# Optimization experiments

Hardware: AMD Instinct MI355X
Metric: run time of the kernel (lower is better)

Reference implementation:

```python
import jax, jax.numpy as jnp
import numpy as np

B, T = 1, 2048
N_HEAD = 16
N_KV_HEAD = 16
N_EMBD = 1024
HEAD_DIM = N_EMBD // N_HEAD  # 64
HD8 = HEAD_DIM // 8          # 8 octonion blocks per head
EPS_RMS = 1e-6


def qconj(q):
    return q * jnp.array([1.0, -1.0, -1.0, -1.0], dtype=q.dtype)


def qmul(q1, q2):
    # Hamilton product, (...,4) x (...,4) -> (...,4)
    w1, x1, y1, z1 = (q1[..., 0], q1[..., 1], q1[..., 2], q1[..., 3])
    w2, x2, y2, z2 = (q2[..., 0], q2[..., 1], q2[..., 2], q2[..., 3])
    return jnp.stack([
        w1 * w2 - x1 * x2 - y1 * y2 - z1 * z2,
        w1 * x2 + x1 * w2 + y1 * z2 - z1 * y2,
        w1 * y2 - x1 * z2 + y1 * w2 + z1 * x2,
        w1 * z2 + x1 * y2 - y1 * x2 + z1 * w2,
    ], axis=-1)


def omul(o1, o2):
    # Cayley-Dickson octonion product, (...,8)
    a, b = o1[..., :4], o1[..., 4:]
    c, d = o2[..., :4], o2[..., 4:]
    first = qmul(a, c) - qmul(qconj(d), b)
    second = qmul(d, a) + qmul(b, qconj(c))
    return jnp.concatenate([first, second], axis=-1)


def oconj(o):
    return jnp.concatenate([qconj(o[..., :4]), -o[..., 4:]], axis=-1)


# Octonion multiplication structure constants: omul(x, y)[k] = x[a] y[p] C[a,p,k]
_EYE8 = jnp.eye(8, dtype=jnp.float32)
C_OCT = jax.vmap(lambda ei: jax.vmap(lambda ej: omul(ei, ej))(_EYE8))(_EYE8)  # (8,8,8)
# Trilinear tensor for omul(omul(q, kc), v):  T3[a,p,q,k] = sum_e C[a,p,e] C[e,q,k]
T3 = jnp.einsum('ape,eqk->apqk', C_OCT, C_OCT)  # (8,8,8,8)


def apply_rotary_emb(x, cos, sin):
    # x: (B, T, H, hd); cos/sin: (1, T, 1, hd//2)
    d = x.shape[-1] // 2
    x1, x2 = x[..., :d], x[..., d:]
    y1 = x1 * cos + x2 * sin
    y2 = x2 * cos - x1 * sin
    return jnp.concatenate([y1, y2], axis=-1)


def rms_norm(x):
    return x * jax.lax.rsqrt(jnp.mean(x * x, axis=-1, keepdims=True) + EPS_RMS)


def setup_inputs() -> dict:
    key = jax.random.key(0)
    ks = jax.random.split(key, 7)
    x = jax.random.normal(ks[0], (B, T, N_EMBD), dtype=jnp.float32)
    cos = jax.random.uniform(ks[1], (1, T, 1, HEAD_DIM // 2), dtype=jnp.float32)
    sin = jax.random.uniform(ks[2], (1, T, 1, HEAD_DIM // 2), dtype=jnp.float32)
    s = 0.02
    Wq = jax.random.normal(ks[3], (N_HEAD * HEAD_DIM, N_EMBD), dtype=jnp.float32) * s
    Wk = jax.random.normal(ks[4], (N_KV_HEAD * HEAD_DIM, N_EMBD), dtype=jnp.float32) * s
    Wv = jax.random.normal(ks[5], (N_KV_HEAD * HEAD_DIM, N_EMBD), dtype=jnp.float32) * s
    Wo = jax.random.normal(ks[6], (N_EMBD, N_EMBD), dtype=jnp.float32) * s
    return {"x": x, "cos": cos, "sin": sin, "Wq": Wq, "Wk": Wk, "Wv": Wv, "Wo": Wo}


def reference(x, cos, sin, Wq, Wk, Wv, Wo):
    Bx, Tx, Cx = x.shape
    q = (x @ Wq.T).reshape(Bx, Tx, N_HEAD, HEAD_DIM)
    k = (x @ Wk.T).reshape(Bx, Tx, N_KV_HEAD, HEAD_DIM)
    v = (x @ Wv.T).reshape(Bx, Tx, N_KV_HEAD, HEAD_DIM)
    q = rms_norm(apply_rotary_emb(q, cos, sin))
    k = rms_norm(apply_rotary_emb(k, cos, sin))
    q = q.transpose(0, 2, 1, 3)  # (B,H,T,hd)
    k = k.transpose(0, 2, 1, 3)
    v = v.transpose(0, 2, 1, 3)

    q_o = q.reshape(Bx, N_HEAD, Tx, HD8, 8)
    k_o = k.reshape(Bx, N_KV_HEAD, Tx, HD8, 8)
    v_o = v.reshape(Bx, N_KV_HEAD, Tx, HD8, 8)
    # F.normalize(p=2, dim=-1): divide by max(||.||, 1e-12)
    k_o = k_o / jnp.maximum(jnp.linalg.norm(k_o, axis=-1, keepdims=True), 1e-12)

    # Scores use the (pre-octonion-normalized) rotary+rms k
    scores = jnp.einsum('bhid,bhjd->bhij', q, k) * (HEAD_DIM ** -0.5)
    mask = jnp.tril(jnp.ones((Tx, Tx), dtype=bool))
    scores = jnp.where(mask, scores, -jnp.inf)
    probs = jax.nn.softmax(scores, axis=-1)  # (B,H,Tq,Tk)

    # y_i = sum_j p_ij * omul(omul(q_i, oconj(k_j)), v_j)
    # omul is bilinear, so pull the j-sum inside:
    # y_i[k] = q_i[a] * T3[a,p,c,k] * (sum_j p_ij kc_j[p] v_j[c])
    kc = oconj(k_o)                                              # (B,H,Tk,M,8)
    KV = jnp.einsum('bhjmp,bhjmq->bhjmpq', kc, v_o)              # (B,H,Tk,M,8,8)
    Z = jnp.einsum('bhij,bhjmpq->bhimpq', probs, KV)             # (B,H,Tq,M,8,8)
    y_o = jnp.einsum('bhima,apqk,bhimpq->bhimk', q_o, T3, Z)     # (B,H,Tq,M,8)

    y = y_o.reshape(Bx, N_HEAD, Tx, HEAD_DIM).transpose(0, 2, 1, 3).reshape(Bx, Tx, Cx)
    return y @ Wo.T
```

## Files before the change

### kernel.cpp

```cpp
#include <hip/hip_runtime.h>

typedef unsigned short u16;
typedef unsigned int u32;

#define T_SEQ 2048
#define NHEAD 16
#define HDIM 64
#define CDIM 1024
#define W_HSTR (512*2048)
#define Z_HSTR (2048*512)
#define P_HSTR 2228224
#define P_TILE 16384

#define SGBITS 0xB2D8741EACC66A00ULL

#define EXP2C 0.18033688011112042f

typedef _Float16 f16x8 __attribute__((ext_vector_type(8)));
typedef float f32x4 __attribute__((ext_vector_type(4)));

__device__ __forceinline__ float h2f(u16 u) { _Float16 h; __builtin_memcpy(&h, &u, 2); return (float)h; }
__device__ __forceinline__ u16 f2h(float f) { _Float16 h = (_Float16)f; u16 u; __builtin_memcpy(&u, &h, 2); return u; }
__device__ __forceinline__ u32 pk(float a, float b) { return (u32)f2h(a) | ((u32)f2h(b) << 16); }

__device__ __forceinline__ void gload16(const u16* g, u16* l) {
    __builtin_amdgcn_global_load_lds((const __attribute__((address_space(1))) u32*)g,
                                     (__attribute__((address_space(3))) u32*)l, 16, 0, 0);
}

template<bool F16OUT>
__device__ __forceinline__ void hgemm_tile(const u16* __restrict__ At, int lda,
                                           const u16* __restrict__ Bt, int ldb, int K,
                                           float* __restrict__ Cf, u16* __restrict__ Ch,
                                           int ldc, float scale, u16* As, u16* Bs) {
    int t = threadIdx.x;
    int wave = t >> 6, l = t & 63;
    int wm = wave & 1, wn = wave >> 1;
    int quad = l >> 4, lr = l & 15;
    f32x4 acc[4][4];
#pragma unroll
    for (int i = 0; i < 4; ++i)
#pragma unroll
        for (int j = 0; j < 4; ++j) acc[i][j] = (f32x4){0.f, 0.f, 0.f, 0.f};
    int acol = quad * 8;
    for (int k0 = 0; k0 < K; k0 += 64) {
#pragma unroll
        for (int j = 0; j < 4; ++j) {
            int d = wave * 4 + j;
            int kb = d >> 3, seg = d & 7;
            size_t roff = (size_t)(seg * 16 + lr);
            int coff = k0 + kb * 32 + acol;
            gload16(At + roff * lda + coff, As + d * 512);
            gload16(Bt + roff * ldb + coff, Bs + d * 512);
        }
        __syncthreads();
#pragma unroll
        for (int kb = 0; kb < 2; ++kb) {
            f16x8 af[4], bf[4];
#pragma unroll
            for (int mi = 0; mi < 4; ++mi) af[mi] = *(const f16x8*)&As[(kb * 8 + wm * 4 + mi) * 512 + l * 8];
#pragma unroll
            for (int ni = 0; ni < 4; ++ni) bf[ni] = *(const f16x8*)&Bs[(kb * 8 + wn * 4 + ni) * 512 + l * 8];
#pragma unroll
            for (int mi = 0; mi < 4; ++mi)
#pragma unroll
                for (int ni = 0; ni < 4; ++ni)
                    acc[mi][ni] = __builtin_amdgcn_mfma_f32_16x16x32_f16(af[mi], bf[ni], acc[mi][ni], 0, 0, 0);
        }
        __syncthreads();
    }
#pragma unroll
    for (int mi = 0; mi < 4; ++mi)
#pragma unroll
        for (int ni = 0; ni < 4; ++ni)
#pragma unroll
            for (int rr = 0; rr < 4; ++rr) {
                int gr = wm * 64 + mi * 16 + quad * 4 + rr;
                int gc = wn * 64 + ni * 16 + lr;
                float v = acc[mi][ni][rr] * scale;
                if (F16OUT) Ch[(size_t)gr * ldc + gc] = f2h(v);
                else Cf[(size_t)gr * ldc + gc] = v;
            }
}

__global__ __launch_bounds__(256) void hgemm_f32(const u16* __restrict__ A, int lda,
                                                 const u16* __restrict__ B, int ldb,
                                                 float* __restrict__ C, int ldc, int K) {
    __shared__ u16 As[8192], Bs[8192];
    int bm = blockIdx.y * 128, bn = blockIdx.x * 128;
    hgemm_tile<false>(A + (size_t)bm * lda, lda, B + (size_t)bn * ldb, ldb, K,
                      C + (size_t)bm * ldc + bn, nullptr, ldc, 1.f, As, Bs);
}

__global__ __launch_bounds__(256) void hgemm_f16(const u16* __restrict__ A, int lda,
                                                 const u16* __restrict__ B, int ldb,
                                                 u16* __restrict__ C, int ldc, int K) {
    __shared__ u16 As[8192], Bs[8192];
    int bm = blockIdx.y * 128, bn = blockIdx.x * 128;
    hgemm_tile<true>(A + (size_t)bm * lda, lda, B + (size_t)bn * ldb, ldb, K,
                     nullptr, C + (size_t)bm * ldc + bn, ldc, 1.f, As, Bs);
}

__global__ __launch_bounds__(256) void qk_exp_p(const u16* __restrict__ q16,
                                                const u16* __restrict__ k16,
                                                u16* __restrict__ P) {
    __shared__ u16 Pt[128 * 144];
    int idx = blockIdx.x;
    int h = idx & 15;
    int tt = idx >> 4;
    int rb = 0;
    while ((rb + 1) * (rb + 2) / 2 <= tt) rb++;
    int cb = tt - rb * (rb + 1) / 2;
    int t = threadIdx.x;
    int wave = t >> 6, l = t & 63;
    int wm = wave & 1, wn = wave >> 1;
    int quad = l >> 4, lr = l & 15;

    const u16* qbase = q16 + (size_t)(rb * 128 + wm * 64 + lr) * CDIM + h * HDIM + quad * 8;
    const u16* kbase = k16 + (size_t)(cb * 128 + wn * 64 + lr) * CDIM + h * HDIM + quad * 8;
    f16x8 qa[4][2], kf[4][2];
#pragma unroll
    for (int mi = 0; mi < 4; ++mi)
#pragma unroll
        for (int kb = 0; kb < 2; ++kb)
            qa[mi][kb] = *(const f16x8*)(qbase + (size_t)(mi * 16) * CDIM + kb * 32);
#pragma unroll
    for (int ni = 0; ni < 4; ++ni)
#pragma unroll
        for (int kb = 0; kb < 2; ++kb)
            kf[ni][kb] = *(const f16x8*)(kbase + (size_t)(ni * 16) * CDIM + kb * 32);

    f32x4 s[4][4];
#pragma unroll
    for (int mi = 0; mi < 4; ++mi)
#pragma unroll
        for (int ni = 0; ni < 4; ++ni) s[mi][ni] = (f32x4){0.f, 0.f, 0.f, 0.f};
#pragma unroll
    for (int kb = 0; kb < 2; ++kb)
#pragma unroll
        for (int mi = 0; mi < 4; ++mi)
#pragma unroll
            for (int ni = 0; ni < 4; ++ni)
                s[mi][ni] = __builtin_amdgcn_mfma_f32_16x16x32_f16(qa[mi][kb], kf[ni][kb], s[mi][ni], 0, 0, 0);

#pragma unroll
    for (int mi = 0; mi < 4; ++mi) {
        int row = wm * 64 + mi * 16 + quad * 4;
#pragma unroll
        for (int ni = 0; ni < 4; ++ni) {
            int col = wn * 64 + ni * 16 + lr;
#pragma unroll
            for (int rr = 0; rr < 4; ++rr) {
                bool valid = (cb < rb) | (col <= row + rr);
                float p = valid ? __builtin_amdgcn_exp2f(s[mi][ni][rr] * EXP2C - 12.f) : 0.f;
                Pt[(row + rr) * 144 + col] = f2h(p);
            }
        }
    }
    __syncthreads();
    u16* Pg = P + (size_t)h * P_HSTR + (size_t)tt * P_TILE;
#pragma unroll
    for (int i = 0; i < 8; ++i) {
        int c = i * 256 + t;
        int row = c >> 4, cw = c & 15;
        uint4 v = *(const uint4*)&Pt[row * 144 + cw * 8];
        *(uint4*)(Pg + row * 128 + cw * 8) = v;
    }
}

__global__ __launch_bounds__(256) void pw_gemm(const u16* __restrict__ P,
                                               const u16* __restrict__ W,
                                               u16* __restrict__ Z,
                                               float* __restrict__ lbuf) {
    __shared__ u16 As[8192], Bs[8192];
    int idx = blockIdx.x;
    int rb = 15 - (idx >> 6);
    int i6 = idx & 63;
    int h = ((i6 & 7) << 1) | ((i6 >> 3) & 1);
    int nq = i6 >> 4;
    int K = (rb + 1) * 128;
    const u16* Ph = P + (size_t)h * P_HSTR + (size_t)(rb * (rb + 1) / 2) * P_TILE;
    const u16* Bt = W + (size_t)h * W_HSTR + (size_t)(nq * 128) * T_SEQ;
    int t = threadIdx.x;
    int wave = t >> 6, l = t & 63;
    int wm = wave & 1, wn = wave >> 1;
    int quad = l >> 4, lr = l & 15;
    int acol = quad * 8;

    f32x4 acc[4][4];
    f32x4 accl[4];
#pragma unroll
    for (int mi = 0; mi < 4; ++mi) {
        accl[mi] = (f32x4){0.f, 0.f, 0.f, 0.f};
#pragma unroll
        for (int ni = 0; ni < 4; ++ni) acc[mi][ni] = (f32x4){0.f, 0.f, 0.f, 0.f};
    }
    f16x8 ones;
#pragma unroll
    for (int j = 0; j < 8; ++j) ones[j] = (_Float16)1.0f;

    for (int k0 = 0; k0 < K; k0 += 64) {
        const u16* At = Ph + (size_t)(k0 >> 7) * P_TILE + (k0 & 64);
#pragma unroll
        for (int j = 0; j < 4; ++j) {
            int d = wave * 4 + j;
            int kb = d >> 3, seg = d & 7;
            size_t roff = (size_t)(seg * 16 + lr);
            gload16(At + roff * 128 + kb * 32 + acol, As + d * 512);
            gload16(Bt + roff * T_SEQ + k0 + kb * 32 + acol, Bs + d * 512);
        }
        __syncthreads();
#pragma unroll
        for (int kb = 0; kb < 2; ++kb) {
            f16x8 af[4], bf[4];
#pragma unroll
            for (int mi = 0; mi < 4; ++mi) af[mi] = *(const f16x8*)&As[(kb * 8 + wm * 4 + mi) * 512 + l * 8];
#pragma unroll
            for (int ni = 0; ni < 4; ++ni) bf[ni] = *(const f16x8*)&Bs[(kb * 8 + wn * 4 + ni) * 512 + l * 8];
#pragma unroll
            for (int mi = 0; mi < 4; ++mi)
#pragma unroll
                for (int ni = 0; ni < 4; ++ni)
                    acc[mi][ni] = __builtin_amdgcn_mfma_f32_16x16x32_f16(af[mi], bf[ni], acc[mi][ni], 0, 0, 0);
            if (nq == 0)
#pragma unroll
                for (int mi = 0; mi < 4; ++mi)
                    accl[mi] = __builtin_amdgcn_mfma_f32_16x16x32_f16(af[mi], ones, accl[mi], 0, 0, 0);
        }
        __syncthreads();
    }

    u16* Zb = Z + (size_t)h * Z_HSTR;
#pragma unroll
    for (int mi = 0; mi < 4; ++mi)
#pragma unroll
        for (int rr = 0; rr < 4; ++rr) {
            int row = rb * 128 + wm * 64 + mi * 16 + quad * 4 + rr;
#pragma unroll
            for (int ni = 0; ni < 4; ++ni) {
                int col = nq * 128 + wn * 64 + ni * 16 + lr;
                Zb[(size_t)row * 512 + col] = f2h(acc[mi][ni][rr]);
            }
        }
    if (nq == 0 && wn == 0 && lr == 0) {
#pragma unroll
        for (int mi = 0; mi < 4; ++mi) {
            int row = rb * 128 + wm * 64 + mi * 16 + quad * 4;
            *(f32x4*)(lbuf + h * T_SEQ + row) = accl[mi];
        }
    }
}

__global__ __launch_bounds__(256) void cvt5(const float* __restrict__ x, const float* __restrict__ wq,
                                            const float* __restrict__ wk, const float* __restrict__ wv,
                                            const float* __restrict__ wo,
                                            u16* __restrict__ x16, u16* __restrict__ w16) {
    int z = blockIdx.y;
    size_t base = ((size_t)blockIdx.x * 256 + threadIdx.x) * 8;
    const float* src;
    u16* dst;
    size_t cnt;
    if (z == 0) { src = x; dst = x16; cnt = 2097152; }
    else if (z == 1) { src = wq; dst = w16; cnt = 1048576; }
    else if (z == 2) { src = wk; dst = w16 + 1048576; cnt = 1048576; }
    else if (z == 3) { src = wv; dst = w16 + 2097152; cnt = 1048576; }
    else { src = wo; dst = w16 + 3145728; cnt = 1048576; }
    if (base >= cnt) return;
    float4 f0 = *(const float4*)(src + base);
    float4 f1 = *(const float4*)(src + base + 4);
    uint4 o;
    o.x = pk(f0.x, f0.y); o.y = pk(f0.z, f0.w); o.z = pk(f1.x, f1.y); o.w = pk(f1.z, f1.w);
    *(uint4*)(dst + base) = o;
}

__global__ __launch_bounds__(256) void prep_rope(const u16* __restrict__ qkv,
                                                 u16* __restrict__ q16, u16* __restrict__ k16,
                                                 float* __restrict__ kc,
                                                 const float* __restrict__ cosb, const float* __restrict__ sinb) {
    int wave = threadIdx.x >> 6, lane = threadIdx.x & 63;
    int idx = blockIdx.x * 4 + wave;
    int t = idx >> 4, h = idx & 15;
    int d = lane & 31;
    float cs = cosb[t * 32 + d];
    float sn = sinb[t * 32 + d];
    size_t b3 = (size_t)t * 3072 + h * HDIM;
    size_t b1 = (size_t)t * CDIM + h * HDIM;

    float xq = h2f(qkv[b3 + lane]);
    float oq = __shfl(xq, lane ^ 32);
    float rq = (lane < 32) ? fmaf(xq, cs, oq * sn) : fmaf(xq, cs, -oq * sn);
    float ssq = rq * rq;
#pragma unroll
    for (int m = 1; m < 64; m <<= 1) ssq += __shfl_xor(ssq, m);
    rq *= rsqrtf(ssq * (1.f / 64.f) + 1e-6f);
    q16[b1 + lane] = f2h(rq);

    float xk = h2f(qkv[b3 + 1024 + lane]);
    float ok = __shfl(xk, lane ^ 32);
    float rk = (lane < 32) ? fmaf(xk, cs, ok * sn) : fmaf(xk, cs, -ok * sn);
    float ssk = rk * rk;
#pragma unroll
    for (int m = 1; m < 64; m <<= 1) ssk += __shfl_xor(ssk, m);
    rk *= rsqrtf(ssk * (1.f / 64.f) + 1e-6f);
    k16[b1 + lane] = f2h(rk);

    float s8 = rk * rk;
    s8 += __shfl_xor(s8, 1); s8 += __shfl_xor(s8, 2); s8 += __shfl_xor(s8, 4);
    float sc2 = 1.f / fmaxf(sqrtf(s8), 1e-12f);
    float kcv = rk * sc2;
    if (lane & 7) kcv = -kcv;
    kc[b1 + lane] = kcv;
}

__global__ __launch_bounds__(256) void w_pre(const float* __restrict__ kc, const u16* __restrict__ qkv,
                                             u16* __restrict__ W) {
    __shared__ float kcs[64][65];
    __shared__ float vs[64][65];
    int h = blockIdx.y;
    int j0 = blockIdx.x * 64;
    int t = threadIdx.x;
    int r = t >> 2, cq = (t & 3) * 16;
    const float* kp = kc + (size_t)(j0 + r) * CDIM + h * HDIM + cq;
    const u16* vp = qkv + (size_t)(j0 + r) * 3072 + 2048 + h * HDIM + cq;
#pragma unroll
    for (int u4 = 0; u4 < 4; ++u4) {
        float4 a = *(const float4*)(kp + u4 * 4);
        ushort4 b = *(const ushort4*)(vp + u4 * 4);
        kcs[r][cq + u4 * 4 + 0] = a.x; kcs[r][cq + u4 * 4 + 1] = a.y;
        kcs[r][cq + u4 * 4 + 2] = a.z; kcs[r][cq + u4 * 4 + 3] = a.w;
        vs[r][cq + u4 * 4 + 0] = h2f(b.x); vs[r][cq + u4 * 4 + 1] = h2f(b.y);
        vs[r][cq + u4 * 4 + 2] = h2f(b.z); vs[r][cq + u4 * 4 + 3] = h2f(b.w);
    }
    __syncthreads();
    int j = t & 63, g = t >> 6;
    u16* Wp = W + (size_t)h * W_HSTR + j0 + j;
    for (int ae = g * 16; ae < g * 16 + 16; ++ae) {
        int a = ae >> 3, e = ae & 7;
        u32 mask = 0;
#pragma unroll
        for (int qq = 0; qq < 8; ++qq) {
            int p = a ^ e ^ qq;
            u32 bit = (u32)(((SGBITS >> (a * 8 + p)) ^ (SGBITS >> ((e ^ qq) * 8 + qq))) & 1ULL);
            mask |= bit << qq;
        }
#pragma unroll
        for (int m = 0; m < 8; ++m) {
            float w = 0.f;
#pragma unroll
            for (int qq = 0; qq < 8; ++qq) {
                float t1 = kcs[j][m * 8 + (a ^ e ^ qq)] * vs[j][m * 8 + qq];
                w = ((mask >> qq) & 1) ? (w - t1) : (w + t1);
            }
            Wp[(size_t)(m * 64 + ae) * T_SEQ] = f2h(w);
        }
    }
}

__global__ __launch_bounds__(256) void contract_y(const u16* __restrict__ q16, const u16* __restrict__ Z,
                                                  const float* __restrict__ lbuf, u16* __restrict__ y16) {
    __shared__ u16 zb[4][512];
    int wave = threadIdx.x >> 6, lane = threadIdx.x & 63;
    int idx = blockIdx.x * 4 + wave;
    int i = idx >> 4, h = idx & 15;
    uint4 zv = *(const uint4*)(Z + (size_t)h * Z_HSTR + (size_t)i * 512 + lane * 8);
    *(uint4*)&zb[wave][lane * 8] = zv;
    int m = lane >> 3, e = lane & 7;
    const u16* qp = q16 + (size_t)i * CDIM + h * HDIM + m * 8;
    uint4 qb = *(const uint4*)qp;
    float qv[8];
    qv[0] = h2f(qb.x & 0xffff); qv[1] = h2f(qb.x >> 16);
    qv[2] = h2f(qb.y & 0xffff); qv[3] = h2f(qb.y >> 16);
    qv[4] = h2f(qb.z & 0xffff); qv[5] = h2f(qb.z >> 16);
    qv[6] = h2f(qb.w & 0xffff); qv[7] = h2f(qb.w >> 16);
    float linv = 1.f / lbuf[h * T_SEQ + i];
    __syncthreads();
    float acc = 0.f;
#pragma unroll
    for (int a = 0; a < 8; ++a) acc = fmaf(qv[a], h2f(zb[wave][m * 64 + a * 8 + e]), acc);
    y16[(size_t)i * CDIM + h * HDIM + lane] = f2h(acc * linv);
}

extern "C" void kernel_launch(void* const* d_in, const int* in_sizes, int n_in,
                              void* d_out, int out_size, void* d_ws, size_t ws_size,
                              hipStream_t stream) {
    const float* x = (const float*)d_in[0];
    const float* cosb = (const float*)d_in[1];
    const float* sinb = (const float*)d_in[2];
    const float* Wq = (const float*)d_in[3];
    const float* Wk = (const float*)d_in[4];
    const float* Wv = (const float*)d_in[5];
    const float* Wo = (const float*)d_in[6];
    float* out = (float*)d_out;
    char* base = (char*)d_ws;
    u16* qkv16 = (u16*)base;
    float* kc = (float*)(base + 12582912);
    u16* x16 = (u16*)(base + 20971520);
    u16* w16 = (u16*)(base + 25165824);
    u16* q16 = (u16*)(base + 33554432);
    u16* k16 = (u16*)(base + 37748736);
    u16* y16 = (u16*)(base + 41943040);
    u16* W = (u16*)(base + 46137344);
    u16* Z = (u16*)(base + 79691776);
    float* lbuf = (float*)(base + 113246208);
    u16* Pbuf = (u16*)(base + 113377280);

    cvt5<<<dim3(1024, 5), 256, 0, stream>>>(x, Wq, Wk, Wv, Wo, x16, w16);
    hgemm_f16<<<dim3(24, 16), 256, 0, stream>>>(x16, CDIM, w16, CDIM, qkv16, 3072, CDIM);
    prep_rope<<<T_SEQ * NHEAD / 4, 256, 0, stream>>>(qkv16, q16, k16, kc, cosb, sinb);
    qk_exp_p<<<16 * 136, 256, 0, stream>>>(q16, k16, Pbuf);
    w_pre<<<dim3(32, 16), 256, 0, stream>>>(kc, qkv16, W);
    pw_gemm<<<1024, 256, 0, stream>>>(Pbuf, W, Z, lbuf);
    contract_y<<<NHEAD * T_SEQ / 4, 256, 0, stream>>>(q16, Z, lbuf, y16);
    hgemm_f32<<<dim3(8, 16), 256, 0, stream>>>(y16, CDIM, w16 + 3145728, CDIM, out, CDIM, CDIM);
}
```

Before: 283.4 us.

## Pair causal row-blocks per workgroup in pw_gemm with 512-thread blocks

The causal P×W GEMM now gives each workgroup two row-blocks, rb=15-jp and rb=jp, so every block does the same total K work. This removes the triangular load imbalance and the tail effect across 1024 uneven blocks. Blocks grow to 512 threads (8 waves), with each wave holding a smaller 32x64 accumulator tile to keep register pressure down. In exchange the grid is halved and jobs run serially inside a block, so per-block latency is longer and occupancy could change.

```diff
diff --git a/kernel.cpp b/kernel.cpp
--- a/kernel.cpp
+++ b/kernel.cpp
@@ -168,85 +168,86 @@
     }
 }
 
-__global__ __launch_bounds__(256) void pw_gemm(const u16* __restrict__ P,
-                                               const u16* __restrict__ W,
-                                               u16* __restrict__ Z,
-                                               float* __restrict__ lbuf) {
+__global__ __launch_bounds__(512, 4) void pw_gemm(const u16* __restrict__ P,
+                                                  const u16* __restrict__ W,
+                                                  u16* __restrict__ Z,
+                                                  float* __restrict__ lbuf) {
     __shared__ u16 As[8192], Bs[8192];
-    int idx = blockIdx.x;
-    int rb = 15 - (idx >> 6);
-    int i6 = idx & 63;
+    int b = blockIdx.x;
+    int jp = b >> 6;
+    int i6 = b & 63;
     int h = ((i6 & 7) << 1) | ((i6 >> 3) & 1);
     int nq = i6 >> 4;
-    int K = (rb + 1) * 128;
-    const u16* Ph = P + (size_t)h * P_HSTR + (size_t)(rb * (rb + 1) / 2) * P_TILE;
     const u16* Bt = W + (size_t)h * W_HSTR + (size_t)(nq * 128) * T_SEQ;
+    u16* Zb = Z + (size_t)h * Z_HSTR;
     int t = threadIdx.x;
     int wave = t >> 6, l = t & 63;
-    int wm = wave & 1, wn = wave >> 1;
+    int wr = wave >> 1, wc = wave & 1;
     int quad = l >> 4, lr = l & 15;
     int acol = quad * 8;
-
-    f32x4 acc[4][4];
-    f32x4 accl[4];
-#pragma unroll
-    for (int mi = 0; mi < 4; ++mi) {
-        accl[mi] = (f32x4){0.f, 0.f, 0.f, 0.f};
-#pragma unroll
-        for (int ni = 0; ni < 4; ++ni) acc[mi][ni] = (f32x4){0.f, 0.f, 0.f, 0.f};
-    }
     f16x8 ones;
 #pragma unroll
     for (int j = 0; j < 8; ++j) ones[j] = (_Float16)1.0f;
 
-    for (int k0 = 0; k0 < K; k0 += 64) {
-        const u16* At = Ph + (size_t)(k0 >> 7) * P_TILE + (k0 & 64);
-#pragma unroll
-        for (int j = 0; j < 4; ++j) {
-            int d = wave * 4 + j;
-            int kb = d >> 3, seg = d & 7;
-            size_t roff = (size_t)(seg * 16 + lr);
-            gload16(At + roff * 128 + kb * 32 + acol, As + d * 512);
-            gload16(Bt + roff * T_SEQ + k0 + kb * 32 + acol, Bs + d * 512);
-        }
-        __syncthreads();
-#pragma unroll
-        for (int kb = 0; kb < 2; ++kb) {
-            f16x8 af[4], bf[4];
-#pragma unroll
-            for (int mi = 0; mi < 4; ++mi) af[mi] = *(const f16x8*)&As[(kb * 8 + wm * 4 + mi) * 512 + l * 8];
-#pragma unroll
-            for (int ni = 0; ni < 4; ++ni) bf[ni] = *(const f16x8*)&Bs[(kb * 8 + wn * 4 + ni) * 512 + l * 8];
-#pragma unroll
-            for (int mi = 0; mi < 4; ++mi)
-#pragma unroll
-                for (int ni = 0; ni < 4; ++ni)
-                    acc[mi][ni] = __builtin_amdgcn_mfma_f32_16x16x32_f16(af[mi], bf[ni], acc[mi][ni], 0, 0, 0);
-            if (nq == 0)
-#pragma unroll
-                for (int mi = 0; mi < 4; ++mi)
-                    accl[mi] = __builtin_amdgcn_mfma_f32_16x16x32_f16(af[mi], ones, accl[mi], 0, 0, 0);
-        }
-        __syncthreads();
-    }
-
-    u16* Zb = Z + (size_t)h * Z_HSTR;
-#pragma unroll
-    for (int mi = 0; mi < 4; ++mi)
-#pragma unroll
-        for (int rr = 0; rr < 4; ++rr) {
-            int row = rb * 128 + wm * 64 + mi * 16 + quad * 4 + rr;
-#pragma unroll
-            for (int ni = 0; ni < 4; ++ni) {
-                int col = nq * 128 + wn * 64 + ni * 16 + lr;
-                Zb[(size_t)row * 512 + col] = f2h(acc[mi][ni][rr]);
-            }
-        }
-    if (nq == 0 && wn == 0 && lr == 0) {
-#pragma unroll
-        for (int mi = 0; mi < 4; ++mi) {
-            int row = rb * 128 + wm * 64 + mi * 16 + quad * 4;
-            *(f32x4*)(lbuf + h * T_SEQ + row) = accl[mi];
+#pragma unroll 1
+    for (int jobi = 0; jobi < 2; ++jobi) {
+        int rb = jobi ? jp : 15 - jp;
+        int K = (rb + 1) * 128;
+        const u16* Ph = P + (size_t)h * P_HSTR + (size_t)(rb * (rb + 1) / 2) * P_TILE;
+        f32x4 acc[2][4];
+        f32x4 accl[2];
+#pragma unroll
+        for (int mi = 0; mi < 2; ++mi) {
+            accl[mi] = (f32x4){0.f, 0.f, 0.f, 0.f};
+#pragma unroll
+            for (int ni = 0; ni < 4; ++ni) acc[mi][ni] = (f32x4){0.f, 0.f, 0.f, 0.f};
+        }
+        for (int k0 = 0; k0 < K; k0 += 64) {
+            const u16* At = Ph + (size_t)(k0 >> 7) * P_TILE + (k0 & 64);
+#pragma unroll
+            for (int j = 0; j < 2; ++j) {
+                int d = wave * 2 + j;
+                int kb = d >> 3, seg = d & 7;
+                size_t roff = (size_t)(seg * 16 + lr);
+                gload16(At + roff * 128 + kb * 32 + acol, As + d * 512);
+                gload16(Bt + roff * T_SEQ + k0 + kb * 32 + acol, Bs + d * 512);
+            }
+            __syncthreads();
+#pragma unroll
+            for (int kb = 0; kb < 2; ++kb) {
+                f16x8 af[2], bf[4];
+#pragma unroll
+                for (int mi = 0; mi < 2; ++mi) af[mi] = *(const f16x8*)&As[(kb * 8 + wr * 2 + mi) * 512 + l * 8];
+#pragma unroll
+                for (int ni = 0; ni < 4; ++ni) bf[ni] = *(const f16x8*)&Bs[(kb * 8 + wc * 4 + ni) * 512 + l * 8];
+#pragma unroll
+                for (int mi = 0; mi < 2; ++mi) {
+#pragma unroll
+                    for (int ni = 0; ni < 4; ++ni)
+                        acc[mi][ni] = __builtin_amdgcn_mfma_f32_16x16x32_f16(af[mi], bf[ni], acc[mi][ni], 0, 0, 0);
+                    if (nq == 0 && wc == 0)
+                        accl[mi] = __builtin_amdgcn_mfma_f32_16x16x32_f16(af[mi], ones, accl[mi], 0, 0, 0);
+                }
+            }
+            __syncthreads();
+        }
+#pragma unroll
+        for (int mi = 0; mi < 2; ++mi)
+#pragma unroll
+            for (int rr = 0; rr < 4; ++rr) {
+                int row = rb * 128 + wr * 32 + mi * 16 + quad * 4 + rr;
+#pragma unroll
+                for (int ni = 0; ni < 4; ++ni) {
+                    int col = nq * 128 + wc * 64 + ni * 16 + lr;
+                    Zb[(size_t)row * 512 + col] = f2h(acc[mi][ni][rr]);
+                }
+            }
+        if (nq == 0 && wc == 0 && lr == 0) {
+#pragma unroll
+            for (int mi = 0; mi < 2; ++mi) {
+                int row = rb * 128 + wr * 32 + mi * 16 + quad * 4;
+                *(f32x4*)(lbuf + h * T_SEQ + row) = accl[mi];
+            }
         }
     }
 }
@@ -409,7 +410,7 @@
     prep_rope<<<T_SEQ * NHEAD / 4, 256, 0, stream>>>(qkv16, q16, k16, kc, cosb, sinb);
     qk_exp_p<<<16 * 136, 256, 0, stream>>>(q16, k16, Pbuf);
     w_pre<<<dim3(32, 16), 256, 0, stream>>>(kc, qkv16, W);
-    pw_gemm<<<1024, 256, 0, stream>>>(Pbuf, W, Z, lbuf);
+    pw_gemm<<<512, 512, 0, stream>>>(Pbuf, W, Z, lbuf);
     contract_y<<<NHEAD * T_SEQ / 4, 256, 0, stream>>>(q16, Z, lbuf, y16);
     hgemm_f32<<<dim3(8, 16), 256, 0, stream>>>(y16, CDIM, w16 + 3145728, CDIM, out, CDIM, CDIM);
 }
```

New measurement: 282.5 us. No clear change (-0.3%).
